# Kernel tuning notes

Measured on AMD Instinct MI355X. Metric: run time of the kernel, lower is better.

The kernel has to match this reference:

```python
import jax, jax.numpy as jnp
import numpy as np

EMBED_DIM = 768
Q_DIM = 64
V_DIM = 64
WINDOW_SIZE = 3


def setup_inputs() -> dict:
    key = jax.random.key(0)
    ks = jax.random.split(key, 7)
    B, N = 4, 4096
    s = 1.0 / np.sqrt(EMBED_DIM)
    x = jax.random.normal(ks[0], (B, N, EMBED_DIM), dtype=jnp.float32)
    Wq = jax.random.normal(ks[1], (EMBED_DIM, Q_DIM), dtype=jnp.float32) * s
    bq = jax.random.normal(ks[2], (Q_DIM,), dtype=jnp.float32) * 0.01
    Wk = jax.random.normal(ks[3], (EMBED_DIM, Q_DIM), dtype=jnp.float32) * s
    bk = jax.random.normal(ks[4], (Q_DIM,), dtype=jnp.float32) * 0.01
    Wv = jax.random.normal(ks[5], (EMBED_DIM, V_DIM), dtype=jnp.float32) * s
    bv = jax.random.normal(ks[6], (V_DIM,), dtype=jnp.float32) * 0.01
    return {"x": x, "Wq": Wq, "bq": bq, "Wk": Wk, "bk": bk, "Wv": Wv, "bv": bv}


def reference(x, Wq, bq, Wk, bk, Wv, bv):
    # Faithful translation of SliddingWindowAttention.forward, including the
    # original's quirk: diagonal scores are written into columns 0..window_size-1
    # of a full (B, N, N) zero matrix, softmax is taken over ALL N columns
    # (zeros included), and the result is matmul'd with V.
    B, N, _ = x.shape
    Q = x @ Wq + bq  # (B, N, Q_DIM)
    K = x @ Wk + bk  # (B, N, Q_DIM)
    V = x @ Wv + bv  # (B, N, V_DIM)

    half = WINDOW_SIZE // 2
    columns = jnp.zeros((B, N, N), dtype=x.dtype)
    for idx, di in enumerate(range(-half, half + 1)):
        # diagonal offset di: pair row i with column j = i + di (valid rows only)
        rows = np.arange(max(0, -di), N - max(0, di))
        cols_j = rows + di
        c = jnp.einsum('bid,bid->bi', Q[:, rows, :], K[:, cols_j, :])
        columns = columns.at[:, rows, idx].set(c)

    attn = jax.nn.softmax(columns, axis=2)  # (B, N, N)
    return attn @ V  # (B, N, V_DIM)
```

## Files before the change

kernel.cpp:

```cpp
#include <hip/hip_runtime.h>
#include <math.h>

#define EMBED 768
#define NTOK  4096
#define NB    4
#define ROWS  16384
#define CN    192

typedef __attribute__((ext_vector_type(8))) short bf16x8;
typedef __attribute__((ext_vector_type(4))) float f32x4;

__device__ inline void split2(float f, short& h, short& l) {
  union { float f; unsigned u; } a; a.f = f;
  unsigned r = (a.u + 0x7FFFu + ((a.u >> 16) & 1u)) & 0xFFFF0000u;
  h = (short)(r >> 16);
  union { unsigned u; float f; } hf; hf.u = r;
  union { float f; unsigned u; } b; b.f = f - hf.f;
  l = (short)((b.u + 0x7FFFu + ((b.u >> 16) & 1u)) >> 16);
}

__global__ __launch_bounds__(256) void wprep(const float* __restrict__ Wq,
                                             const float* __restrict__ Wk,
                                             const float* __restrict__ Wv,
                                             unsigned short* __restrict__ Wt) {
  int t = blockIdx.x * 256 + threadIdx.x;
  int n = t / 768, k = t - n * 768;
  float w;
  if (n < 64)        w = Wq[k * 64 + n];
  else if (n < 128)  w = Wk[k * 64 + (n - 64)];
  else               w = Wv[k * 64 + (n - 128)];
  short h, l; split2(w, h, l);
  Wt[(size_t)n * 768 + k]         = (unsigned short)h;
  Wt[(size_t)(192 + n) * 768 + k] = (unsigned short)l;
}

__global__ __launch_bounds__(128) void qkv_mfma(const float* __restrict__ x,
                                                const unsigned short* __restrict__ Wtu,
                                                const float* __restrict__ bq,
                                                const float* __restrict__ bk,
                                                const float* __restrict__ bv,
                                                float* __restrict__ C) {
  const int lane = threadIdx.x & 63;
  const int wn   = threadIdx.x >> 6;
  const int ml   = lane & 15;
  const int q    = lane >> 4;
  const int r0   = blockIdx.x * 32;
  const int nbase = wn * 96;

  f32x4 acc[2][6] = {};

  const float* xa0 = x + (size_t)(r0 + ml) * EMBED + q * 8;
  const float* xa1 = x + (size_t)(r0 + 16 + ml) * EMBED + q * 8;
  const bf16x8* wt = (const bf16x8*)Wtu;

  int bidx[12];
#pragma unroll
  for (int p = 0; p < 2; ++p)
#pragma unroll
    for (int nt = 0; nt < 6; ++nt)
      bidx[p * 6 + nt] = (p * 192 + nbase + nt * 16 + ml) * 96 + q;

  float4 ca[4]; bf16x8 cb[12];
  ca[0] = *(const float4*)(xa0);     ca[1] = *(const float4*)(xa0 + 4);
  ca[2] = *(const float4*)(xa1);     ca[3] = *(const float4*)(xa1 + 4);
#pragma unroll
  for (int j = 0; j < 12; ++j) cb[j] = wt[bidx[j]];

  for (int ks = 0; ks < 24; ++ks) {
    float4 na[4]; bf16x8 nb[12];
    if (ks < 23) {
      const float* p0 = xa0 + (ks + 1) * 32;
      const float* p1 = xa1 + (ks + 1) * 32;
      na[0] = *(const float4*)(p0);  na[1] = *(const float4*)(p0 + 4);
      na[2] = *(const float4*)(p1);  na[3] = *(const float4*)(p1 + 4);
#pragma unroll
      for (int j = 0; j < 12; ++j) nb[j] = wt[bidx[j] + (ks + 1) * 4];
    }

    bf16x8 ah0, al0, ah1, al1;
    {
      float f0[8] = {ca[0].x, ca[0].y, ca[0].z, ca[0].w,
                     ca[1].x, ca[1].y, ca[1].z, ca[1].w};
      float f1[8] = {ca[2].x, ca[2].y, ca[2].z, ca[2].w,
                     ca[3].x, ca[3].y, ca[3].z, ca[3].w};
#pragma unroll
      for (int j = 0; j < 8; ++j) {
        short h, l;
        split2(f0[j], h, l); ah0[j] = h; al0[j] = l;
        split2(f1[j], h, l); ah1[j] = h; al1[j] = l;
      }
    }

#pragma unroll
    for (int nt = 0; nt < 6; ++nt) {
      bf16x8 bh = cb[nt], bl = cb[6 + nt];
      acc[0][nt] = __builtin_amdgcn_mfma_f32_16x16x32_bf16(ah0, bh, acc[0][nt], 0, 0, 0);
      acc[0][nt] = __builtin_amdgcn_mfma_f32_16x16x32_bf16(ah0, bl, acc[0][nt], 0, 0, 0);
      acc[0][nt] = __builtin_amdgcn_mfma_f32_16x16x32_bf16(al0, bh, acc[0][nt], 0, 0, 0);
      acc[1][nt] = __builtin_amdgcn_mfma_f32_16x16x32_bf16(ah1, bh, acc[1][nt], 0, 0, 0);
      acc[1][nt] = __builtin_amdgcn_mfma_f32_16x16x32_bf16(ah1, bl, acc[1][nt], 0, 0, 0);
      acc[1][nt] = __builtin_amdgcn_mfma_f32_16x16x32_bf16(al1, bh, acc[1][nt], 0, 0, 0);
    }

#pragma unroll
    for (int j = 0; j < 4; ++j)  ca[j] = na[j];
#pragma unroll
    for (int j = 0; j < 12; ++j) cb[j] = nb[j];
  }

#pragma unroll
  for (int nt = 0; nt < 6; ++nt) {
    int n = nbase + nt * 16 + ml;
    float bias = (n < 64) ? bq[n] : (n < 128) ? bk[n - 64] : bv[n - 128];
#pragma unroll
    for (int mt = 0; mt < 2; ++mt) {
#pragma unroll
      for (int reg = 0; reg < 4; ++reg) {
        int row = r0 + mt * 16 + q * 4 + reg;
        C[(size_t)row * CN + n] = acc[mt][nt][reg] + bias;
      }
    }
  }
}

__global__ __launch_bounds__(256) void vsum_kernel(const float* __restrict__ C,
                                                   float* __restrict__ Vsum) {
  __shared__ float red[4][64];
  const int t = threadIdx.x;
  const int d = t & 63;
  const int g = t >> 6;
  const int batch = blockIdx.x >> 6;
  const int chunk = blockIdx.x & 63;
  const size_t base =
      ((size_t)batch * NTOK + (size_t)chunk * 64 + (size_t)g * 16) * CN + 128 + d;
  float s = 0.f;
#pragma unroll
  for (int rr = 0; rr < 16; ++rr) s += C[base + (size_t)rr * CN];
  red[g][d] = s;
  __syncthreads();
  if (g == 0) {
    atomicAdd(&Vsum[batch * 64 + d],
              red[0][d] + red[1][d] + red[2][d] + red[3][d]);
  }
}

__global__ __launch_bounds__(256) void attn_kernel(const float* __restrict__ C,
                                                   const float* __restrict__ Vsum,
                                                   float* __restrict__ out) {
  const int t    = threadIdx.x;
  const int lane = t & 63;
  const int wave = t >> 6;
  const int r = blockIdx.x * 4 + wave;
  const int b = r >> 12;
  const int i = r & (NTOK - 1);

  const float q  = C[(size_t)r * CN + lane];
  const float kc = C[(size_t)r * CN + 64 + lane];
  float km = 0.f, kp = 0.f;
  if (i > 0)        km = C[(size_t)(r - 1) * CN + 64 + lane];
  if (i < NTOK - 1) kp = C[(size_t)(r + 1) * CN + 64 + lane];

  float p0 = q * km, p1 = q * kc, p2 = q * kp;
#pragma unroll
  for (int off = 32; off > 0; off >>= 1) {
    p0 += __shfl_xor(p0, off, 64);
    p1 += __shfl_xor(p1, off, 64);
    p2 += __shfl_xor(p2, off, 64);
  }

  const float s0 = (i > 0) ? p0 : 0.f;
  const float s1 = p1;
  const float s2 = (i < NTOK - 1) ? p2 : 0.f;
  const float m  = fmaxf(fmaxf(s0, s1), fmaxf(s2, 0.f));
  const float e0 = expf(s0 - m);
  const float e1 = expf(s1 - m);
  const float e2 = expf(s2 - m);
  const float ez = expf(-m);
  const float Z  = e0 + e1 + e2 + (float)(NTOK - 3) * ez;

  const size_t vb = ((size_t)b * NTOK) * CN + 128;
  const float v0 = C[vb + lane];
  const float v1 = C[vb + CN + lane];
  const float v2 = C[vb + 2 * (size_t)CN + lane];
  const float vs = Vsum[b * 64 + lane];

  out[(size_t)r * 64 + lane] =
      (e0 * v0 + e1 * v1 + e2 * v2 + ez * (vs - v0 - v1 - v2)) / Z;
}

extern "C" void kernel_launch(void* const* d_in, const int* in_sizes, int n_in,
                              void* d_out, int out_size, void* d_ws, size_t ws_size,
                              hipStream_t stream) {
  const float* x  = (const float*)d_in[0];
  const float* Wq = (const float*)d_in[1];
  const float* bq = (const float*)d_in[2];
  const float* Wk = (const float*)d_in[3];
  const float* bk = (const float*)d_in[4];
  const float* Wv = (const float*)d_in[5];
  const float* bv = (const float*)d_in[6];
  float* out = (float*)d_out;

  float* C    = (float*)d_ws;
  float* Vsum = C + (size_t)ROWS * CN;
  unsigned short* Wt = (unsigned short*)(Vsum + NB * 64);

  hipMemsetAsync(Vsum, 0, NB * 64 * sizeof(float), stream);
  wprep<<<576, 256, 0, stream>>>(Wq, Wk, Wv, Wt);
  qkv_mfma<<<512, 128, 0, stream>>>(x, Wt, bq, bk, bv, C);
  vsum_kernel<<<256, 256, 0, stream>>>(C, Vsum);
  attn_kernel<<<ROWS / 4, 256, 0, stream>>>(C, Vsum, out);
}
```

Baseline: 148.7 us.

## Fuse V column sum into QKV GEMM and re-tile weight layout

The Vsum reduction moves into the QKV MFMA epilogue, where per-wave V column sums are taken via shuffles and atomics, so the separate vsum kernel and its extra read of C go away. The memset is folded into wprep. wprep now transposes through shared memory into a k-slab-major layout (32-wide k chunks) with vectorized stores. The GEMM uses 256-thread blocks with each wave owning a 16-row tile, plus double-buffered register prefetch. In exchange, each wave does less work per loaded weight fragment, and correctness depends on wprep finishing the Vsum zeroing before the GEMM atomics run.

```diff
diff --git a/kernel.cpp b/kernel.cpp
--- a/kernel.cpp
+++ b/kernel.cpp
@@ -8,6 +8,7 @@
 #define CN    192
 
 typedef __attribute__((ext_vector_type(8))) short bf16x8;
+typedef __attribute__((ext_vector_type(8))) unsigned short u16x8;
 typedef __attribute__((ext_vector_type(4))) float f32x4;
 
 __device__ inline void split2(float f, short& h, short& l) {
@@ -22,125 +23,138 @@
 __global__ __launch_bounds__(256) void wprep(const float* __restrict__ Wq,
                                              const float* __restrict__ Wk,
                                              const float* __restrict__ Wv,
-                                             unsigned short* __restrict__ Wt) {
-  int t = blockIdx.x * 256 + threadIdx.x;
-  int n = t / 768, k = t - n * 768;
-  float w;
-  if (n < 64)        w = Wq[k * 64 + n];
-  else if (n < 128)  w = Wk[k * 64 + (n - 64)];
-  else               w = Wv[k * 64 + (n - 128)];
-  short h, l; split2(w, h, l);
-  Wt[(size_t)n * 768 + k]         = (unsigned short)h;
-  Wt[(size_t)(192 + n) * 768 + k] = (unsigned short)l;
-}
-
-__global__ __launch_bounds__(128) void qkv_mfma(const float* __restrict__ x,
-                                                const unsigned short* __restrict__ Wtu,
-                                                const float* __restrict__ bq,
-                                                const float* __restrict__ bk,
-                                                const float* __restrict__ bv,
-                                                float* __restrict__ C) {
-  const int lane = threadIdx.x & 63;
-  const int wn   = threadIdx.x >> 6;
-  const int ml   = lane & 15;
-  const int q    = lane >> 4;
-  const int r0   = blockIdx.x * 32;
+                                             unsigned short* __restrict__ Wt,
+                                             float* __restrict__ Vsum) {
+  __shared__ float tile[32 * 64];
+  const int b   = blockIdx.x;
+  const int mat = b / 24;
+  const int ks  = b - mat * 24;
+  const float* W = (mat == 0) ? Wq : (mat == 1) ? Wk : Wv;
+  const int t = threadIdx.x;
+
+  const float4* src = (const float4*)(W + ks * 2048);
+  ((float4*)tile)[t]       = src[t];
+  ((float4*)tile)[t + 256] = src[t + 256];
+  __syncthreads();
+
+  const int n  = t >> 2;
+  const int ko = (t & 3) * 8;
+  u16x8 hv, lv;
+#pragma unroll
+  for (int j = 0; j < 8; ++j) {
+    short h, l;
+    split2(tile[(ko + j) * 64 + n], h, l);
+    hv[j] = (unsigned short)h;
+    lv[j] = (unsigned short)l;
+  }
+  const size_t base = (size_t)ks * 12288 + (size_t)(mat * 64 + n) * 32 + ko;
+  *(u16x8*)(Wt + base)        = hv;
+  *(u16x8*)(Wt + base + 6144) = lv;
+
+  if (b == 0 && t < NB * 64) Vsum[t] = 0.f;
+}
+
+__device__ inline void cvt8(const float4 a0, const float4 a1, bf16x8& h, bf16x8& l) {
+  const float f[8] = {a0.x, a0.y, a0.z, a0.w, a1.x, a1.y, a1.z, a1.w};
+#pragma unroll
+  for (int j = 0; j < 8; ++j) {
+    union { float f; unsigned u; } a; a.f = f[j];
+    unsigned th = a.u + 0x7FFFu + ((a.u >> 16) & 1u);
+    h[j] = (short)(th >> 16);
+    union { unsigned u; float f; } hf; hf.u = th & 0xFFFF0000u;
+    union { float f; unsigned u; } r; r.f = f[j] - hf.f;
+    unsigned tl = r.u + 0x7FFFu + ((r.u >> 16) & 1u);
+    l[j] = (short)(tl >> 16);
+  }
+}
+
+__device__ inline void loadA(const float* __restrict__ p, float4* d) {
+  d[0] = *(const float4*)p;
+  d[1] = *(const float4*)(p + 4);
+}
+
+__device__ inline void loadB(const unsigned short* __restrict__ p0,
+                             const unsigned short* __restrict__ p1, bf16x8* d) {
+#pragma unroll
+  for (int nt = 0; nt < 6; ++nt) {
+    d[nt]     = *(const bf16x8*)(p0 + (nt - 2) * 512);
+    d[6 + nt] = *(const bf16x8*)(p1 + (nt - 2) * 512);
+  }
+}
+
+__device__ inline void compute6(const float4* A, const bf16x8* B, f32x4* acc) {
+  bf16x8 ah, al;
+  cvt8(A[0], A[1], ah, al);
+#pragma unroll
+  for (int nt = 0; nt < 6; ++nt) {
+    acc[nt] = __builtin_amdgcn_mfma_f32_16x16x32_bf16(ah, B[nt],     acc[nt], 0, 0, 0);
+    acc[nt] = __builtin_amdgcn_mfma_f32_16x16x32_bf16(ah, B[6 + nt], acc[nt], 0, 0, 0);
+    acc[nt] = __builtin_amdgcn_mfma_f32_16x16x32_bf16(al, B[nt],     acc[nt], 0, 0, 0);
+  }
+}
+
+__global__ __launch_bounds__(256, 2) void qkv_mfma(const float* __restrict__ x,
+                                                   const unsigned short* __restrict__ Wtu,
+                                                   const float* __restrict__ bq,
+                                                   const float* __restrict__ bk,
+                                                   const float* __restrict__ bv,
+                                                   float* __restrict__ C,
+                                                   float* __restrict__ Vsum) {
+  const int lane  = threadIdx.x & 63;
+  const int wm    = (threadIdx.x >> 6) & 1;
+  const int wn    = threadIdx.x >> 7;
+  const int ml    = lane & 15;
+  const int q     = lane >> 4;
+  const int r0    = blockIdx.x * 32;
   const int nbase = wn * 96;
 
-  f32x4 acc[2][6] = {};
-
-  const float* xa0 = x + (size_t)(r0 + ml) * EMBED + q * 8;
-  const float* xa1 = x + (size_t)(r0 + 16 + ml) * EMBED + q * 8;
-  const bf16x8* wt = (const bf16x8*)Wtu;
-
-  int bidx[12];
-#pragma unroll
-  for (int p = 0; p < 2; ++p)
-#pragma unroll
-    for (int nt = 0; nt < 6; ++nt)
-      bidx[p * 6 + nt] = (p * 192 + nbase + nt * 16 + ml) * 96 + q;
-
-  float4 ca[4]; bf16x8 cb[12];
-  ca[0] = *(const float4*)(xa0);     ca[1] = *(const float4*)(xa0 + 4);
-  ca[2] = *(const float4*)(xa1);     ca[3] = *(const float4*)(xa1 + 4);
-#pragma unroll
-  for (int j = 0; j < 12; ++j) cb[j] = wt[bidx[j]];
-
-  for (int ks = 0; ks < 24; ++ks) {
-    float4 na[4]; bf16x8 nb[12];
-    if (ks < 23) {
-      const float* p0 = xa0 + (ks + 1) * 32;
-      const float* p1 = xa1 + (ks + 1) * 32;
-      na[0] = *(const float4*)(p0);  na[1] = *(const float4*)(p0 + 4);
-      na[2] = *(const float4*)(p1);  na[3] = *(const float4*)(p1 + 4);
-#pragma unroll
-      for (int j = 0; j < 12; ++j) nb[j] = wt[bidx[j] + (ks + 1) * 4];
+  f32x4 acc[6] = {};
+
+  const float* xap = x + (size_t)(r0 + wm * 16 + ml) * EMBED + q * 8;
+  const unsigned short* b0 = Wtu + (nbase + 32 + ml) * 32 + q * 8;
+  const unsigned short* b1 = b0 + 6144;
+
+  float4 A0[2], A1[2];
+  bf16x8 B0[12], B1[12];
+
+  loadA(xap, A0);
+  loadB(b0, b1, B0);
+  b0 += 12288; b1 += 12288;
+
+  for (int ks = 0; ks < 24; ks += 2) {
+    loadA(xap + 32, A1);
+    loadB(b0, b1, B1);
+    b0 += 12288; b1 += 12288;
+    compute6(A0, B0, acc);
+    if (ks < 22) {
+      loadA(xap + 64, A0);
+      loadB(b0, b1, B0);
+      b0 += 12288; b1 += 12288;
     }
-
-    bf16x8 ah0, al0, ah1, al1;
-    {
-      float f0[8] = {ca[0].x, ca[0].y, ca[0].z, ca[0].w,
-                     ca[1].x, ca[1].y, ca[1].z, ca[1].w};
-      float f1[8] = {ca[2].x, ca[2].y, ca[2].z, ca[2].w,
-                     ca[3].x, ca[3].y, ca[3].z, ca[3].w};
-#pragma unroll
-      for (int j = 0; j < 8; ++j) {
-        short h, l;
-        split2(f0[j], h, l); ah0[j] = h; al0[j] = l;
-        split2(f1[j], h, l); ah1[j] = h; al1[j] = l;
-      }
+    xap += 64;
+    compute6(A1, B1, acc);
+  }
+
+#pragma unroll
+  for (int nt = 0; nt < 6; ++nt) {
+    const int n = nbase + nt * 16 + ml;
+    const float bias = (n < 64) ? bq[n] : (n < 128) ? bk[n - 64] : bv[n - 128];
+#pragma unroll
+    for (int reg = 0; reg < 4; ++reg) {
+      const int row = r0 + wm * 16 + q * 4 + reg;
+      C[(size_t)row * CN + n] = acc[nt][reg] + bias;
     }
-
-#pragma unroll
-    for (int nt = 0; nt < 6; ++nt) {
-      bf16x8 bh = cb[nt], bl = cb[6 + nt];
-      acc[0][nt] = __builtin_amdgcn_mfma_f32_16x16x32_bf16(ah0, bh, acc[0][nt], 0, 0, 0);
-      acc[0][nt] = __builtin_amdgcn_mfma_f32_16x16x32_bf16(ah0, bl, acc[0][nt], 0, 0, 0);
-      acc[0][nt] = __builtin_amdgcn_mfma_f32_16x16x32_bf16(al0, bh, acc[0][nt], 0, 0, 0);
-      acc[1][nt] = __builtin_amdgcn_mfma_f32_16x16x32_bf16(ah1, bh, acc[1][nt], 0, 0, 0);
-      acc[1][nt] = __builtin_amdgcn_mfma_f32_16x16x32_bf16(ah1, bl, acc[1][nt], 0, 0, 0);
-      acc[1][nt] = __builtin_amdgcn_mfma_f32_16x16x32_bf16(al1, bh, acc[1][nt], 0, 0, 0);
+  }
+
+  if (wn == 1) {
+#pragma unroll
+    for (int nt = 2; nt < 6; ++nt) {
+      const int n = nbase + nt * 16 + ml;
+      float s = acc[nt][0] + acc[nt][1] + acc[nt][2] + acc[nt][3] + 4.f * bv[n - 128];
+      s += __shfl_xor(s, 16, 64);
+      s += __shfl_xor(s, 32, 64);
+      if (q == 0) atomicAdd(&Vsum[(r0 >> 12) * 64 + (n - 128)], s);
     }
-
-#pragma unroll
-    for (int j = 0; j < 4; ++j)  ca[j] = na[j];
-#pragma unroll
-    for (int j = 0; j < 12; ++j) cb[j] = nb[j];
-  }
-
-#pragma unroll
-  for (int nt = 0; nt < 6; ++nt) {
-    int n = nbase + nt * 16 + ml;
-    float bias = (n < 64) ? bq[n] : (n < 128) ? bk[n - 64] : bv[n - 128];
-#pragma unroll
-    for (int mt = 0; mt < 2; ++mt) {
-#pragma unroll
-      for (int reg = 0; reg < 4; ++reg) {
-        int row = r0 + mt * 16 + q * 4 + reg;
-        C[(size_t)row * CN + n] = acc[mt][nt][reg] + bias;
-      }
-    }
-  }
-}
-
-__global__ __launch_bounds__(256) void vsum_kernel(const float* __restrict__ C,
-                                                   float* __restrict__ Vsum) {
-  __shared__ float red[4][64];
-  const int t = threadIdx.x;
-  const int d = t & 63;
-  const int g = t >> 6;
-  const int batch = blockIdx.x >> 6;
-  const int chunk = blockIdx.x & 63;
-  const size_t base =
-      ((size_t)batch * NTOK + (size_t)chunk * 64 + (size_t)g * 16) * CN + 128 + d;
-  float s = 0.f;
-#pragma unroll
-  for (int rr = 0; rr < 16; ++rr) s += C[base + (size_t)rr * CN];
-  red[g][d] = s;
-  __syncthreads();
-  if (g == 0) {
-    atomicAdd(&Vsum[batch * 64 + d],
-              red[0][d] + red[1][d] + red[2][d] + red[3][d]);
   }
 }
 
@@ -204,9 +218,7 @@
   float* Vsum = C + (size_t)ROWS * CN;
   unsigned short* Wt = (unsigned short*)(Vsum + NB * 64);
 
-  hipMemsetAsync(Vsum, 0, NB * 64 * sizeof(float), stream);
-  wprep<<<576, 256, 0, stream>>>(Wq, Wk, Wv, Wt);
-  qkv_mfma<<<512, 128, 0, stream>>>(x, Wt, bq, bk, bv, C);
-  vsum_kernel<<<256, 256, 0, stream>>>(C, Vsum);
+  wprep<<<72, 256, 0, stream>>>(Wq, Wk, Wv, Wt, Vsum);
+  qkv_mfma<<<512, 256, 0, stream>>>(x, Wt, bq, bk, bv, C, Vsum);
   attn_kernel<<<ROWS / 4, 256, 0, stream>>>(C, Vsum, out);
 }
```

After: 143.9 us. -3.3%, faster.
